# Kernel optimization log

Hardware: AMD Instinct MI355X
Metric: run time of the kernel (lower is better)

## Reference

```python
import jax, jax.numpy as jnp
import numpy as np

EMB = 64          # emb_size
LG = 64           # lg_msg_dim
NDB = 16          # num_dist_basis
NCB = 16          # num_cos_basis
NCLS = 40
NLAYERS = 2
NJK = NLAYERS + 2  # jumping-knowledge sequence length
HID = (NJK * EMB) // 2  # PyG JK-LSTM hidden size = 128


def setup_inputs() -> dict:
    key = jax.random.key(0)
    ks = jax.random.split(key, 24)
    N, Eg, Elg, F = 50000, 800000, 800000, 128
    s = 0.05
    inp = {
        "x": jax.random.normal(ks[0], (N, F), jnp.float32),
        "edge_index_g": jax.random.randint(ks[1], (2, Eg), 0, N, jnp.int32),
        "edge_attr_g": jax.random.uniform(ks[2], (Eg, NDB), jnp.float32),
        "edge_index_lg": jax.random.randint(ks[3], (2, Elg), 0, Eg, jnp.int32),
        "edge_attr_lg": jax.random.uniform(ks[4], (Elg, NCB), jnp.float32),
        # parameters (nn.Linear convention: W is [out, in])
        "W_feat": jax.random.normal(ks[5], (EMB, F), jnp.float32) * s,
        "W_msg": jax.random.normal(ks[6], (LG, 2 * EMB + NDB), jnp.float32) * s,
        "W_lg2g": jax.random.normal(ks[7], (EMB, LG), jnp.float32) * s,
        "b_lg2g": jax.random.normal(ks[8], (EMB,), jnp.float32) * s,
        "W_msg_layers": jax.random.normal(ks[9], (NLAYERS, LG, 2 * LG + NCB), jnp.float32) * s,
        # bidirectional LSTM params (PyTorch gate order i,f,g,o)
        "Wih_f": jax.random.normal(ks[10], (4 * HID, EMB), jnp.float32) * s,
        "Whh_f": jax.random.normal(ks[11], (4 * HID, HID), jnp.float32) * s,
        "bih_f": jax.random.normal(ks[12], (4 * HID,), jnp.float32) * s,
        "bhh_f": jax.random.normal(ks[13], (4 * HID,), jnp.float32) * s,
        "Wih_b": jax.random.normal(ks[14], (4 * HID, EMB), jnp.float32) * s,
        "Whh_b": jax.random.normal(ks[15], (4 * HID, HID), jnp.float32) * s,
        "bih_b": jax.random.normal(ks[16], (4 * HID,), jnp.float32) * s,
        "bhh_b": jax.random.normal(ks[17], (4 * HID,), jnp.float32) * s,
        "W_att": jax.random.normal(ks[18], (1, 2 * HID), jnp.float32) * s,
        "b_att": jax.random.normal(ks[19], (1,), jnp.float32) * s,
        "W_out": jax.random.normal(ks[20], (NCLS, EMB), jnp.float32) * s,
    }
    return inp


def _lstm(x_seq, Wih, Whh, bih, bhh, reverse):
    # x_seq: [N, L, C] -> hs: [N, L, H]
    N = x_seq.shape[0]
    H = Whh.shape[1]
    b = bih + bhh

    def step(carry, x_t):
        h, c = carry
        gates = x_t @ Wih.T + h @ Whh.T + b
        i, f, g, o = jnp.split(gates, 4, axis=-1)
        c = jax.nn.sigmoid(f) * c + jax.nn.sigmoid(i) * jnp.tanh(g)
        h = jax.nn.sigmoid(o) * jnp.tanh(c)
        return (h, c), h

    xs = jnp.swapaxes(x_seq, 0, 1)  # [L, N, C]
    init = (jnp.zeros((N, H), x_seq.dtype), jnp.zeros((N, H), x_seq.dtype))
    _, hs = jax.lax.scan(step, init, xs, reverse=reverse)
    return jnp.swapaxes(hs, 0, 1)


def reference(x, edge_index_g, edge_attr_g, edge_index_lg, edge_attr_lg,
              W_feat, W_msg, W_lg2g, b_lg2g, W_msg_layers,
              Wih_f, Whh_f, bih_f, bhh_f, Wih_b, Whh_b, bih_b, bhh_b,
              W_att, b_att, W_out):
    N = x.shape[0]
    Eg = edge_attr_g.shape[0]
    seg = jax.ops.segment_sum

    # node embedding (eval mode: dropout is identity)
    node_emb = jax.nn.relu(x @ W_feat.T)  # [N, EMB]

    # initial linegraph node features: gather endpoints -> concat -> linear -> relu
    m1 = node_emb[edge_index_g[0]]  # [Eg, EMB]
    m2 = node_emb[edge_index_g[1]]
    msg_emb = jax.nn.relu(jnp.concatenate([m1, m2, edge_attr_g], -1) @ W_msg.T)  # [Eg, LG]

    node_embs = [node_emb]
    msg_red = msg_emb @ W_lg2g.T + b_lg2g
    node_embs.append(seg(msg_red, edge_index_g[1], num_segments=N))

    # message-passing layers on the linegraph
    for l in range(W_msg_layers.shape[0]):
        s = msg_emb[edge_index_lg[0]]
        d = msg_emb[edge_index_lg[1]]
        m = jax.nn.relu(jnp.concatenate([s, d, edge_attr_lg], -1) @ W_msg_layers[l].T)
        msg_emb = seg(m, edge_index_lg[1], num_segments=Eg)  # scatter_add over linegraph
        incoming = seg(msg_emb, edge_index_g[1], num_segments=N)
        node_embs.append(incoming @ W_lg2g.T + b_lg2g)

    # JumpingKnowledge ('lstm'): bidirectional LSTM -> attention -> weighted sum
    x_jk = jnp.stack(node_embs, axis=1)  # [N, NJK, EMB]
    h_f = _lstm(x_jk, Wih_f, Whh_f, bih_f, bhh_f, reverse=False)
    h_b = _lstm(x_jk, Wih_b, Whh_b, bih_b, bhh_b, reverse=True)
    h = jnp.concatenate([h_f, h_b], -1)  # [N, NJK, 2*HID]
    alpha = jax.nn.softmax((h @ W_att.T + b_att)[..., 0], axis=-1)  # [N, NJK]
    final_emb = jnp.sum(x_jk * alpha[..., None], axis=1)  # [N, EMB]

    out = final_emb @ W_out.T
    return jax.nn.log_softmax(out, axis=-1)
```

## Files before the change

### kernel.cpp

```cpp
#include <hip/hip_runtime.h>

typedef unsigned short u16;
typedef unsigned int u32;
typedef __attribute__((ext_vector_type(8))) short bf16x8;
typedef __attribute__((ext_vector_type(4))) float f32x4;

#define MFMA(a, b, c) __builtin_amdgcn_mfma_f32_16x16x32_bf16(a, b, c, 0, 0, 0)

__device__ __forceinline__ u16 f2bf(float x) {
    union { float f; u32 u; } v; v.f = x;
    u32 r = (v.u + 0x7FFFu + ((v.u >> 16) & 1u)) >> 16;
    return (u16)r;
}
__device__ __forceinline__ float bf2f(u16 b) {
    union { u32 u; float f; } v; v.u = ((u32)b) << 16;
    return v.f;
}
__device__ __forceinline__ void casAddPair(u32* w, float lo, float hi) {
    u32 old = *w, assumed;
    do {
        assumed = old;
        u32 des = (u32)f2bf(bf2f((u16)(assumed & 0xFFFFu)) + lo) |
                  ((u32)f2bf(bf2f((u16)(assumed >> 16)) + hi) << 16);
        if (des == assumed) break;
        old = atomicCAS(w, assumed, des);
    } while (old != assumed);
}

__global__ __launch_bounds__(256) void prep_w(
    const float* __restrict__ Whh_f, const float* __restrict__ Whh_b,
    const float* __restrict__ Wih_f, const float* __restrict__ Wih_b,
    const float* __restrict__ bih_f, const float* __restrict__ bhh_f,
    const float* __restrict__ bih_b, const float* __restrict__ bhh_b,
    u16* __restrict__ WhhB, u16* __restrict__ WihB, float* __restrict__ BS)
{
    const float L2E = 1.4426950408889634f;
    int i = blockIdx.x * 256 + threadIdx.x;
    if (i < 131072) {
        int d = i >> 16, r = i & 65535;
        float s = (((r >> 14) & 3) == 2) ? 2.f * L2E : L2E;
        WhhB[i] = f2bf(s * (d ? Whh_b[r] : Whh_f[r]));
    } else if (i < 196608) {
        int i2 = i - 131072; int d = i2 >> 15, r = i2 & 32767;
        float s = (((r >> 13) & 3) == 2) ? 2.f * L2E : L2E;
        WihB[i2] = f2bf(s * (d ? Wih_b[r] : Wih_f[r]));
    } else if (i < 197632) {
        int i3 = i - 196608; int d = i3 >> 9, g = i3 & 511;
        float s = (((g >> 7) & 3) == 2) ? 2.f * L2E : L2E;
        BS[i3] = s * (d ? (bih_b[g] + bhh_b[g]) : (bih_f[g] + bhh_f[g]));
    }
}

__global__ __launch_bounds__(256) void count_kernel(const int* __restrict__ dst,
                                                    u32* __restrict__ cnt, long E)
{
    long i = (long)blockIdx.x * 256 + threadIdx.x;
    if (i < E) atomicAdd(&cnt[dst[i]], 1u);
}

__global__ __launch_bounds__(256) void scan1(const u32* __restrict__ a,
                                             u32* __restrict__ part, int n)
{
    __shared__ u32 ts[256];
    int b = blockIdx.x, t = threadIdx.x;
    long i0 = (long)b * 1024 + t * 4;
    u32 s = 0;
#pragma unroll
    for (int k = 0; k < 4; ++k) { long i = i0 + k; if (i < n) s += a[i]; }
    ts[t] = s; __syncthreads();
    for (int off = 1; off < 256; off <<= 1) {
        u32 x = (t >= off) ? ts[t - off] : 0u;
        __syncthreads(); ts[t] += x; __syncthreads();
    }
    if (t == 255) part[b] = ts[255];
}

__global__ __launch_bounds__(1024) void scan2(u32* __restrict__ part, int nb,
                                              u32* __restrict__ total_out)
{
    __shared__ u32 ts[1024];
    int t = threadIdx.x;
    u32 v = (t < nb) ? part[t] : 0u;
    ts[t] = v; __syncthreads();
    for (int off = 1; off < 1024; off <<= 1) {
        u32 x = (t >= off) ? ts[t - off] : 0u;
        __syncthreads(); ts[t] += x; __syncthreads();
    }
    if (t < nb) part[t] = ts[t] - v;
    if (t == 1023 && total_out) *total_out = ts[1023];
}

__global__ __launch_bounds__(256) void scan3(u32* __restrict__ a,
                                             const u32* __restrict__ part, int n)
{
    __shared__ u32 ts[256];
    int b = blockIdx.x, t = threadIdx.x;
    long i0 = (long)b * 1024 + t * 4;
    u32 v[4]; u32 s = 0;
#pragma unroll
    for (int k = 0; k < 4; ++k) { long i = i0 + k; v[k] = (i < n) ? a[i] : 0u; s += v[k]; }
    ts[t] = s; __syncthreads();
    for (int off = 1; off < 256; off <<= 1) {
        u32 x = (t >= off) ? ts[t - off] : 0u;
        __syncthreads(); ts[t] += x; __syncthreads();
    }
    u32 run = part[b] + ts[t] - s;
#pragma unroll
    for (int k = 0; k < 4; ++k) {
        long i = i0 + k;
        if (i < n) { u32 x = v[k]; a[i] = run; run += x; }
    }
}

__global__ __launch_bounds__(256) void fill_kernel(const int* __restrict__ dst,
                                                   u32* __restrict__ off,
                                                   int* __restrict__ list, long E)
{
    long i = (long)blockIdx.x * 256 + threadIdx.x;
    if (i < E) {
        u32 pos = atomicAdd(&off[dst[i]], 1u);
        list[pos] = (int)i;
    }
}

__global__ __launch_bounds__(256) void zero_fill(const u32* __restrict__ offc,
                                                 u16* __restrict__ outb, long NB)
{
    long idx = (long)blockIdx.x * 256 + threadIdx.x;
    long n = idx >> 3; int q = (int)(idx & 7);
    if (n >= NB) return;
    u32 s = n ? offc[n - 1] : 0u;
    u32 e = offc[n];
    bool need = (s == e) || ((s >> 7) != ((e - 1) >> 7));
    if (need) *(uint4*)(outb + n * 64 + q * 8) = make_uint4(0, 0, 0, 0);
}

template <int K, bool RELU, bool INBF16>
__global__ __launch_bounds__(256) void rowgemm(
    const void* __restrict__ in, const float* __restrict__ W,
    const float* __restrict__ bias, const float* __restrict__ bias_scale,
    u16* __restrict__ outb, int M)
{
    constexpr int KP = K + 8;
    __shared__ u16 inS[64 * KP];
    __shared__ u16 WS[64 * KP];
    int t = threadIdx.x;
    long rb = (long)blockIdx.x * 64;
    for (int i = t; i < 64 * K; i += 256) {
        int c = i / K, k = i - c * K;
        WS[c * KP + k] = f2bf(W[i]);
    }
    if (INBF16) {
        const u16* inb = (const u16*)in;
        for (int i = t; i < 64 * K / 8; i += 256) {
            int r = i / (K / 8), q = i - r * (K / 8);
            long gr = rb + r;
            uint4 v = make_uint4(0, 0, 0, 0);
            if (gr < M) v = *(const uint4*)&inb[gr * (long)K + q * 8];
            *(uint4*)&inS[r * KP + q * 8] = v;
        }
    } else {
        const float* inf = (const float*)in;
        for (int i = t; i < 64 * K; i += 256) {
            int r = i / K, k = i - r * K;
            long gr = rb + r;
            inS[r * KP + k] = (gr < M) ? f2bf(inf[gr * (long)K + k]) : (u16)0;
        }
    }
    __syncthreads();
    int l = t & 63, w = t >> 6, lr = l & 15, lq = l >> 4;
    f32x4 acc[4];
#pragma unroll
    for (int i = 0; i < 4; ++i) acc[i] = (f32x4){0.f, 0.f, 0.f, 0.f};
#pragma unroll
    for (int kc = 0; kc < K; kc += 32) {
        bf16x8 a = *(const bf16x8*)&inS[(w * 16 + lr) * KP + kc + lq * 8];
#pragma unroll
        for (int ct = 0; ct < 4; ++ct) {
            bf16x8 b = *(const bf16x8*)&WS[(ct * 16 + lr) * KP + kc + lq * 8];
            acc[ct] = MFMA(a, b, acc[ct]);
        }
    }
#pragma unroll
    for (int ct = 0; ct < 4; ++ct)
#pragma unroll
        for (int r = 0; r < 4; ++r) {
            long gr = rb + w * 16 + lq * 4 + r;
            if (gr < M) {
                int c = ct * 16 + lr;
                float v = acc[ct][r];
                if (bias) v += bias[c] * (bias_scale ? bias_scale[gr] : 1.f);
                if (RELU) v = fmaxf(v, 0.f);
                outb[gr * 64 + c] = f2bf(v);
            }
        }
}

__global__ __launch_bounds__(512, 4) void edge_msg_init2(
    const u16* __restrict__ feat, const int* __restrict__ ei,
    const float* __restrict__ attr, const float* __restrict__ W,
    u16* __restrict__ outb, long E)
{
    __shared__ u16 WS[64 * 168];
    __shared__ u16 eds[128 * 64];
    int t = threadIdx.x;
    long eb = (long)blockIdx.x * 128;
    for (int i = t; i < 64 * 144; i += 512) {
        int c = i / 144, k = i - c * 144;
        WS[c * 168 + k] = f2bf(W[i]);
    }
    for (int i = t; i < 64 * 24; i += 512) {
        int c = i / 24, k = 144 + (i - c * 24);
        WS[c * 168 + k] = 0;
    }
    int w = t >> 6, l = t & 63, lr = l & 15, lq = l >> 4;
    long e = eb + w * 16 + lr;
    long ec = (e < E) ? e : (E - 1);
    int src = ei[ec], dst = ei[E + ec];
    bf16x8 A[5];
    {
        const uint4* sp = (const uint4*)(feat + (long)src * 64);
        const uint4* dp = (const uint4*)(feat + (long)dst * 64);
        *(uint4*)&A[0] = sp[lq];
        *(uint4*)&A[1] = sp[4 + lq];
        *(uint4*)&A[2] = dp[lq];
        *(uint4*)&A[3] = dp[4 + lq];
        uint4 pv = make_uint4(0, 0, 0, 0);
        if (lq < 2) {
            const float4* ap = (const float4*)(attr + ec * 16) + lq * 2;
            float4 b0 = ap[0], b1 = ap[1];
            pv.x = (u32)f2bf(b0.x) | ((u32)f2bf(b0.y) << 16);
            pv.y = (u32)f2bf(b0.z) | ((u32)f2bf(b0.w) << 16);
            pv.z = (u32)f2bf(b1.x) | ((u32)f2bf(b1.y) << 16);
            pv.w = (u32)f2bf(b1.z) | ((u32)f2bf(b1.w) << 16);
        }
        *(uint4*)&A[4] = pv;
    }
    __syncthreads();
    f32x4 acc[4];
#pragma unroll
    for (int ct = 0; ct < 4; ++ct) acc[ct] = (f32x4){0.f, 0.f, 0.f, 0.f};
#pragma unroll
    for (int kc = 0; kc < 5; ++kc) {
#pragma unroll
        for (int ct = 0; ct < 4; ++ct) {
            bf16x8 b = *(const bf16x8*)&WS[(ct * 16 + lr) * 168 + kc * 32 + lq * 8];
            acc[ct] = MFMA(A[kc], b, acc[ct]);
        }
    }
#pragma unroll
    for (int ct = 0; ct < 4; ++ct)
#pragma unroll
        for (int r = 0; r < 4; ++r) {
            int row = w * 16 + lq * 4 + r;
            int col = ct * 16 + lr;
            eds[row * 64 + col] = f2bf(fmaxf(acc[ct][r], 0.f));
        }
    __syncthreads();
    for (int j = t; j < 1024; j += 512) {
        int le = j >> 3, q = j & 7;
        long e2 = eb + le;
        if (e2 < E)
            *(uint4*)(outb + e2 * 64 + q * 8) = *(const uint4*)&eds[le * 64 + q * 8];
    }
}

__global__ __launch_bounds__(512, 4) void edge_msg_lg2(
    const u16* __restrict__ feat, const int* __restrict__ ei,
    const float* __restrict__ attr, const float* __restrict__ W,
    const int* __restrict__ list, u16* __restrict__ outb, long E)
{
    __shared__ u16 WS[64 * 168];
    __shared__ u16 eds[128 * 64];
    __shared__ int dstS[128];
    __shared__ int idS[128];
    __shared__ int srcS[128];
    __shared__ int dprevS, dnextS;
    int t = threadIdx.x;
    long pb = (long)blockIdx.x * 128;
    for (int i = t; i < 64 * 144; i += 512) {
        int c = i / 144, k = i - c * 144;
        WS[c * 168 + k] = f2bf(W[i]);
    }
    for (int i = t; i < 64 * 24; i += 512) {
        int c = i / 24, k = 144 + (i - c * 24);
        WS[c * 168 + k] = 0;
    }
    if (t < 128) {
        long p = pb + t;
        int id = (p < E) ? list[p] : -1;
        idS[t] = id;
        srcS[t] = (id >= 0) ? ei[id] : 0;
        dstS[t] = (id >= 0) ? ei[E + id] : -1;
    } else if (t == 128) {
        dprevS = (pb > 0) ? ei[E + list[pb - 1]] : -2;
    } else if (t == 129) {
        dnextS = (pb + 128 < E) ? ei[E + list[pb + 128]] : -2;
    }
    __syncthreads();
    int w = t >> 6, l = t & 63, lr = l & 15, lq = l >> 4;
    int el = w * 16 + lr;
    int id = idS[el];
    long idc = (id >= 0) ? (long)id : 0;
    int src = srcS[el];
    int dst = (dstS[el] >= 0) ? dstS[el] : 0;
    bf16x8 A[5];
    {
        const uint4* sp = (const uint4*)(feat + (long)src * 64);
        const uint4* dp = (const uint4*)(feat + (long)dst * 64);
        *(uint4*)&A[0] = sp[lq];
        *(uint4*)&A[1] = sp[4 + lq];
        *(uint4*)&A[2] = dp[lq];
        *(uint4*)&A[3] = dp[4 + lq];
        uint4 pv = make_uint4(0, 0, 0, 0);
        if (lq < 2) {
            const float4* ap = (const float4*)(attr + idc * 16) + lq * 2;
            float4 b0 = ap[0], b1 = ap[1];
            pv.x = (u32)f2bf(b0.x) | ((u32)f2bf(b0.y) << 16);
            pv.y = (u32)f2bf(b0.z) | ((u32)f2bf(b0.w) << 16);
            pv.z = (u32)f2bf(b1.x) | ((u32)f2bf(b1.y) << 16);
            pv.w = (u32)f2bf(b1.z) | ((u32)f2bf(b1.w) << 16);
        }
        *(uint4*)&A[4] = pv;
    }
    f32x4 acc[4];
#pragma unroll
    for (int ct = 0; ct < 4; ++ct) acc[ct] = (f32x4){0.f, 0.f, 0.f, 0.f};
#pragma unroll
    for (int kc = 0; kc < 5; ++kc) {
#pragma unroll
        for (int ct = 0; ct < 4; ++ct) {
            bf16x8 b = *(const bf16x8*)&WS[(ct * 16 + lr) * 168 + kc * 32 + lq * 8];
            acc[ct] = MFMA(A[kc], b, acc[ct]);
        }
    }
#pragma unroll
    for (int ct = 0; ct < 4; ++ct)
#pragma unroll
        for (int r = 0; r < 4; ++r) {
            int row = w * 16 + lq * 4 + r;
            int col = ct * 16 + lr;
            eds[row * 64 + col] = f2bf(fmaxf(acc[ct][r], 0.f));
        }
    __syncthreads();
    for (int j = t; j < 4096; j += 512) {
        int le = j >> 5, wd = j & 31;
        int d = dstS[le];
        if (d < 0) continue;
        if (le > 0 && dstS[le - 1] == d) continue;
        float lo = 0.f, hi = 0.f;
        int le2 = le;
        do {
            u32 pair = *(const u32*)&eds[le2 * 64 + wd * 2];
            lo += bf2f((u16)(pair & 0xFFFFu));
            hi += bf2f((u16)(pair >> 16));
            ++le2;
        } while (le2 < 128 && dstS[le2] == d);
        bool bprev = (le == 0 && dprevS == d);
        bool bnext = (le2 == 128 && dnextS == d);
        u32* dw = (u32*)(outb + (long)d * 64 + wd * 2);
        if (bprev || bnext) {
            casAddPair(dw, lo, hi);
        } else {
            *dw = (u32)f2bf(lo) | ((u32)f2bf(hi) << 16);
        }
    }
}

__global__ __launch_bounds__(256) void gather_g(
    const u16* __restrict__ m, const int* __restrict__ list,
    const u32* __restrict__ offc, u16* __restrict__ aggB,
    float* __restrict__ degOut, int N)
{
    int t = threadIdx.x;
    int hw = t >> 5, c = t & 31;
    long n = (long)blockIdx.x * 8 + hw;
    if (n >= N) return;
    u32 start = n ? offc[n - 1] : 0u;
    u32 end = offc[n];
    float s0 = 0.f, s1 = 0.f;
    for (u32 i = start; i < end; ++i) {
        int e = list[i];
        u32 pair = *(const u32*)&m[(long)e * 64 + c * 2];
        s0 += bf2f((u16)(pair & 0xFFFFu));
        s1 += bf2f((u16)(pair >> 16));
    }
    *(u32*)&aggB[n * 64 + c * 2] = (u32)f2bf(s0) | ((u32)f2bf(s1) << 16);
    if (degOut && c == 0) degOut[n] = (float)(end - start);
}

__global__ __launch_bounds__(512, 2) void lstm3(
    const u16* __restrict__ jkB, const u16* __restrict__ WhhB,
    const u16* __restrict__ WihB, const float* __restrict__ BS,
    const float* __restrict__ Watt, float* __restrict__ scores,
    int N)
{
    __shared__ u16 hS[64 * 136];
    __shared__ u16 xS[4][64 * 72];
    __shared__ u16 WiS[512 * 72];
    __shared__ float bsS[512];
    __shared__ float part[4 * 64 * 8];
    int t = threadIdx.x;
    int dir = blockIdx.y;
    int w = t >> 6, l = t & 63, lr = l & 15, lq = l >> 4;
    const u16* WhhD = WhhB + (long)dir * 65536;
    const u16* WihD = WihB + (long)dir * 32768;
    long n0 = (long)blockIdx.x * 64;

    {
        int n = t >> 3, j = t & 7;
        long gn = n0 + n;
#pragma unroll
        for (int k = 0; k < 4; ++k) {
            uint4 v = make_uint4(0, 0, 0, 0);
            if (gn < N) v = *(const uint4*)&jkB[((long)k * N + gn) * 64 + j * 8];
            *(uint4*)&xS[k][n * 72 + j * 8] = v;
        }
    }
#pragma unroll
    for (int i = t; i < 4096; i += 512) {
        int g = i >> 3, q = i & 7;
        *(uint4*)&WiS[g * 72 + q * 8] = *(const uint4*)&WihD[g * 64 + q * 8];
    }
    bsS[t] = BS[dir * 512 + t];

    int grow0 = w * 16 + lq * 4;
    bf16x8 Wh[4][4];
#pragma unroll
    for (int ty = 0; ty < 4; ++ty) {
        int g = ty * 128 + w * 16 + lr;
#pragma unroll
        for (int kc = 0; kc < 4; ++kc)
            Wh[ty][kc] = *(const bf16x8*)&WhhD[g * 128 + kc * 32 + lq * 8];
    }
    float4 Wa4 = *(const float4*)&Watt[dir * 128 + grow0];
    float* scOut = scores + (long)dir * N * 4;

    float creg[4][4] = {};
    __syncthreads();

#pragma unroll 1
    for (int s = 0; s < 4; ++s) {
        int tt = dir ? (3 - s) : s;
        float u[4][4];
        {
            f32x4 acc[2][4];
            f32x4 bi = *(const f32x4*)&bsS[grow0];
            f32x4 bg = *(const f32x4*)&bsS[256 + grow0];
#pragma unroll
            for (int nt = 0; nt < 4; ++nt) { acc[0][nt] = bi; acc[1][nt] = bg; }
            if (s) {
#pragma unroll
                for (int kc = 0; kc < 4; ++kc) {
                    bf16x8 a[4];
#pragma unroll
                    for (int nt = 0; nt < 4; ++nt)
                        a[nt] = *(const bf16x8*)&hS[(nt * 16 + lr) * 136 + kc * 32 + lq * 8];
#pragma unroll
                    for (int nt = 0; nt < 4; ++nt) {
                        acc[0][nt] = MFMA(Wh[0][kc], a[nt], acc[0][nt]);
                        acc[1][nt] = MFMA(Wh[2][kc], a[nt], acc[1][nt]);
                    }
                }
            }
#pragma unroll
            for (int kc = 0; kc < 2; ++kc) {
                bf16x8 wi = *(const bf16x8*)&WiS[(w * 16 + lr) * 72 + kc * 32 + lq * 8];
                bf16x8 wg = *(const bf16x8*)&WiS[(256 + w * 16 + lr) * 72 + kc * 32 + lq * 8];
                bf16x8 a[4];
#pragma unroll
                for (int nt = 0; nt < 4; ++nt)
                    a[nt] = *(const bf16x8*)&xS[tt][(nt * 16 + lr) * 72 + kc * 32 + lq * 8];
#pragma unroll
                for (int nt = 0; nt < 4; ++nt) {
                    acc[0][nt] = MFMA(wi, a[nt], acc[0][nt]);
                    acc[1][nt] = MFMA(wg, a[nt], acc[1][nt]);
                }
            }
#pragma unroll
            for (int nt = 0; nt < 4; ++nt)
#pragma unroll
                for (int r = 0; r < 4; ++r) {
                    float si = __builtin_amdgcn_rcpf(
                        1.f + __builtin_amdgcn_exp2f(-acc[0][nt][r]));
                    float tg = 2.f * __builtin_amdgcn_rcpf(
                        1.f + __builtin_amdgcn_exp2f(-acc[1][nt][r])) - 1.f;
                    u[nt][r] = si * tg;
                }
        }
        {
            f32x4 acc[2][4];
            f32x4 bf = *(const f32x4*)&bsS[128 + grow0];
            f32x4 bo = *(const f32x4*)&bsS[384 + grow0];
#pragma unroll
            for (int nt = 0; nt < 4; ++nt) { acc[0][nt] = bf; acc[1][nt] = bo; }
            if (s) {
#pragma unroll
                for (int kc = 0; kc < 4; ++kc) {
                    bf16x8 a[4];
#pragma unroll
                    for (int nt = 0; nt < 4; ++nt)
                        a[nt] = *(const bf16x8*)&hS[(nt * 16 + lr) * 136 + kc * 32 + lq * 8];
#pragma unroll
                    for (int nt = 0; nt < 4; ++nt) {
                        acc[0][nt] = MFMA(Wh[1][kc], a[nt], acc[0][nt]);
                        acc[1][nt] = MFMA(Wh[3][kc], a[nt], acc[1][nt]);
                    }
                }
            }
#pragma unroll
            for (int kc = 0; kc < 2; ++kc) {
                bf16x8 wf = *(const bf16x8*)&WiS[(128 + w * 16 + lr) * 72 + kc * 32 + lq * 8];
                bf16x8 wo = *(const bf16x8*)&WiS[(384 + w * 16 + lr) * 72 + kc * 32 + lq * 8];
                bf16x8 a[4];
#pragma unroll
                for (int nt = 0; nt < 4; ++nt)
                    a[nt] = *(const bf16x8*)&xS[tt][(nt * 16 + lr) * 72 + kc * 32 + lq * 8];
#pragma unroll
                for (int nt = 0; nt < 4; ++nt) {
                    acc[0][nt] = MFMA(wf, a[nt], acc[0][nt]);
                    acc[1][nt] = MFMA(wo, a[nt], acc[1][nt]);
                }
            }
            if (s) __syncthreads();
#pragma unroll
            for (int nt = 0; nt < 4; ++nt) {
                float hv[4];
#pragma unroll
                for (int r = 0; r < 4; ++r) {
                    float sf = __builtin_amdgcn_rcpf(
                        1.f + __builtin_amdgcn_exp2f(-acc[0][nt][r]));
                    float c = sf * creg[nt][r] + u[nt][r];
                    float so = __builtin_amdgcn_rcpf(
                        1.f + __builtin_amdgcn_exp2f(-acc[1][nt][r]));
                    float th = 2.f * __builtin_amdgcn_rcpf(
                        1.f + __builtin_amdgcn_exp2f(-2.8853900817779268f * c)) - 1.f;
                    creg[nt][r] = c;
                    hv[r] = so * th;
                }
                float p = hv[0] * Wa4.x + hv[1] * Wa4.y + hv[2] * Wa4.z + hv[3] * Wa4.w;
                p += __shfl_xor(p, 16);
                p += __shfl_xor(p, 32);
                if (lq == 0) part[(tt * 64 + nt * 16 + lr) * 8 + w] = p;
                if (s < 3) {
                    u32 p0 = (u32)f2bf(hv[0]) | ((u32)f2bf(hv[1]) << 16);
                    u32 p1 = (u32)f2bf(hv[2]) | ((u32)f2bf(hv[3]) << 16);
                    *(uint2*)&hS[(nt * 16 + lr) * 136 + grow0] = make_uint2(p0, p1);
                }
            }
        }
        if (s < 3) __syncthreads();
    }
    __syncthreads();
    if (t < 256) {
        int tt = t >> 6, node = t & 63;
        long gn = n0 + node;
        if (gn < N) {
            const float4* pp = (const float4*)&part[(tt * 64 + node) * 8];
            float4 a = pp[0], b = pp[1];
            scOut[gn * 4 + tt] = a.x + a.y + a.z + a.w + b.x + b.y + b.z + b.w;
        }
    }
}

__global__ __launch_bounds__(256) void final_kernel(
    const u16* __restrict__ jkB, const float* __restrict__ scores,
    const float* __restrict__ Wout, float* __restrict__ out, int N)
{
    __shared__ float feS[4][64];
    int t = threadIdx.x, l = t & 63, w = t >> 6;
    long n = (long)blockIdx.x * 4 + w;
    bool ok = (n < N);
    long nn = ok ? n : (long)(N - 1);
    float sc[4];
#pragma unroll
    for (int tt = 0; tt < 4; ++tt)
        sc[tt] = scores[nn * 4 + tt] + scores[(long)N * 4 + nn * 4 + tt];
    float m = fmaxf(fmaxf(sc[0], sc[1]), fmaxf(sc[2], sc[3]));
    float e0 = __expf(sc[0] - m), e1 = __expf(sc[1] - m);
    float e2 = __expf(sc[2] - m), e3 = __expf(sc[3] - m);
    float den = e0 + e1 + e2 + e3;
    float a0 = e0 / den, a1 = e1 / den, a2 = e2 / den, a3 = e3 / den;
    float fe = a0 * bf2f(jkB[nn * 64 + l]) + a1 * bf2f(jkB[((long)N + nn) * 64 + l]) +
               a2 * bf2f(jkB[((long)2 * N + nn) * 64 + l]) +
               a3 * bf2f(jkB[((long)3 * N + nn) * 64 + l]);
    feS[w][l] = fe;
    __syncthreads();
    float logit = 0.f;
    if (l < 40)
        for (int c = 0; c < 64; ++c) logit += feS[w][c] * Wout[l * 64 + c];
    float v = (l < 40) ? logit : -1e30f;
    for (int off = 32; off; off >>= 1) v = fmaxf(v, __shfl_xor(v, off));
    float ex = (l < 40) ? __expf(logit - v) : 0.f;
    for (int off = 32; off; off >>= 1) ex += __shfl_xor(ex, off);
    if (ok && l < 40) out[n * 40 + l] = logit - v - __logf(ex);
}

extern "C" void kernel_launch(void* const* d_in, const int* in_sizes, int n_in,
                              void* d_out, int out_size, void* d_ws, size_t ws_size,
                              hipStream_t stream)
{
    const float* x        = (const float*)d_in[0];
    const int*   eig      = (const int*)d_in[1];
    const float* eag      = (const float*)d_in[2];
    const int*   eilg     = (const int*)d_in[3];
    const float* ealg     = (const float*)d_in[4];
    const float* W_feat   = (const float*)d_in[5];
    const float* W_msg    = (const float*)d_in[6];
    const float* W_lg2g   = (const float*)d_in[7];
    const float* b_lg2g   = (const float*)d_in[8];
    const float* W_msg_l  = (const float*)d_in[9];
    const float* Wih_f    = (const float*)d_in[10];
    const float* Whh_f    = (const float*)d_in[11];
    const float* bih_f    = (const float*)d_in[12];
    const float* bhh_f    = (const float*)d_in[13];
    const float* Wih_b    = (const float*)d_in[14];
    const float* Whh_b    = (const float*)d_in[15];
    const float* bih_b    = (const float*)d_in[16];
    const float* bhh_b    = (const float*)d_in[17];
    const float* W_att    = (const float*)d_in[18];
    const float* W_out    = (const float*)d_in[20];

    int  N   = in_sizes[0] / 128;
    long Eg  = in_sizes[1] / 2;
    long Elg = in_sizes[3] / 2;

    char* wp = (char*)d_ws;
    auto alloc = [&](size_t bytes) -> char* {
        char* p = wp; wp += (bytes + 255) & ~(size_t)255; return p;
    };
    u16*   jkB    = (u16*)  alloc((size_t)4 * N * 64 * 2);
    u16*   mA     = (u16*)  alloc((size_t)Eg * 64 * 2);
    u16*   mB     = (u16*)  alloc((size_t)Eg * 64 * 2);
    u16*   aggB   = (u16*)  alloc((size_t)N * 64 * 2);
    float* deg    = (float*)alloc((size_t)N * 4);
    float* scores = (float*)alloc((size_t)2 * N * 4 * 4);
    u16*   WhhB   = (u16*)  alloc((size_t)2 * 65536 * 2);
    u16*   WihB   = (u16*)  alloc((size_t)2 * 32768 * 2);
    float* BS     = (float*)alloc((size_t)2 * 512 * 4);
    u32*   off_g  = (u32*)  alloc((size_t)(N + 1) * 4);
    int*   list_g = (int*)  alloc((size_t)Eg * 4);
    u32*   off_lg = (u32*)  alloc((size_t)(Eg + 1) * 4);
    int*   list_lg= (int*)  alloc((size_t)Elg * 4);
    u32*   part   = (u32*)  alloc((size_t)1024 * 4);

    prep_w<<<772, 256, 0, stream>>>(Whh_f, Whh_b, Wih_f, Wih_b,
                                    bih_f, bhh_f, bih_b, bhh_b, WhhB, WihB, BS);
    hipMemsetAsync(off_g, 0, (size_t)(N + 1) * 4, stream);
    count_kernel<<<(int)((Eg + 255) / 256), 256, 0, stream>>>(eig + Eg, off_g, Eg);
    {
        int nb = (N + 1023) / 1024;
        scan1<<<nb, 256, 0, stream>>>(off_g, part, N);
        scan2<<<1, 1024, 0, stream>>>(part, nb, off_g + N);
        scan3<<<nb, 256, 0, stream>>>(off_g, part, N);
    }
    fill_kernel<<<(int)((Eg + 255) / 256), 256, 0, stream>>>(eig + Eg, off_g, list_g, Eg);
    hipMemsetAsync(off_lg, 0, (size_t)(Eg + 1) * 4, stream);
    count_kernel<<<(int)((Elg + 255) / 256), 256, 0, stream>>>(eilg + Elg, off_lg, Elg);
    {
        int nb = (int)((Eg + 1023) / 1024);
        scan1<<<nb, 256, 0, stream>>>(off_lg, part, (int)Eg);
        scan2<<<1, 1024, 0, stream>>>(part, nb, off_lg + Eg);
        scan3<<<nb, 256, 0, stream>>>(off_lg, part, (int)Eg);
    }
    fill_kernel<<<(int)((Elg + 255) / 256), 256, 0, stream>>>(eilg + Elg, off_lg, list_lg, Elg);

    rowgemm<128, true, false><<<(N + 63) / 64, 256, 0, stream>>>(
        x, W_feat, nullptr, nullptr, jkB, N);
    edge_msg_init2<<<(int)((Eg + 127) / 128), 512, 0, stream>>>(
        jkB, eig, eag, W_msg, mA, Eg);
    gather_g<<<(N + 7) / 8, 256, 0, stream>>>(mA, list_g, off_g, aggB, deg, N);
    rowgemm<64, false, true><<<(N + 63) / 64, 256, 0, stream>>>(
        aggB, W_lg2g, b_lg2g, deg, jkB + (size_t)N * 64, N);
    zero_fill<<<(int)((Eg * 8 + 255) / 256), 256, 0, stream>>>(off_lg, mB, Eg);
    edge_msg_lg2<<<(int)((Elg + 127) / 128), 512, 0, stream>>>(
        mA, eilg, ealg, W_msg_l, list_lg, mB, Elg);
    gather_g<<<(N + 7) / 8, 256, 0, stream>>>(mB, list_g, off_g, aggB, nullptr, N);
    rowgemm<64, false, true><<<(N + 63) / 64, 256, 0, stream>>>(
        aggB, W_lg2g, b_lg2g, nullptr, jkB + (size_t)2 * N * 64, N);
    zero_fill<<<(int)((Eg * 8 + 255) / 256), 256, 0, stream>>>(off_lg, mA, Eg);
    edge_msg_lg2<<<(int)((Elg + 127) / 128), 512, 0, stream>>>(
        mB, eilg, ealg, W_msg_l + 64 * 144, list_lg, mA, Elg);
    gather_g<<<(N + 7) / 8, 256, 0, stream>>>(mA, list_g, off_g, aggB, nullptr, N);
    rowgemm<64, false, true><<<(N + 63) / 64, 256, 0, stream>>>(
        aggB, W_lg2g, b_lg2g, nullptr, jkB + (size_t)3 * N * 64, N);
    {
        int ntiles = (N + 63) / 64;
        lstm3<<<dim3(ntiles, 2), 512, 0, stream>>>(
            jkB, WhhB, WihB, BS, W_att, scores, N);
    }
    final_kernel<<<(N + 3) / 4, 256, 0, stream>>>(
        jkB, scores, W_out, (float*)d_out, N);
}
```

Baseline: 1.061 ms.

## Pre-convert weights to bf16 once, split gather across two half-waves, slim LSTM LDS

Weight matrices for the feature, message and lg2g GEMMs are now converted to bf16 once in prep_w, and the edge and row GEMM kernels load them with vectorized 16-byte copies instead of converting fp32 per block. gather_g assigns one full wave per node, with each half-wave summing alternate edges before a shuffle reduction, which doubles parallelism on high-degree nodes. The LSTM kernel drops its input-weight and bias LDS staging, reads them from global or cache into registers, adds the biases before the activations, and raises the occupancy hint to 4. Packed bf16 conversion instructions replace the manual rounding, adding a few extra global loads per step in exchange.

```diff
diff --git a/kernel.cpp b/kernel.cpp
--- a/kernel.cpp
+++ b/kernel.cpp
@@ -32,7 +32,11 @@
     const float* __restrict__ Wih_f, const float* __restrict__ Wih_b,
     const float* __restrict__ bih_f, const float* __restrict__ bhh_f,
     const float* __restrict__ bih_b, const float* __restrict__ bhh_b,
-    u16* __restrict__ WhhB, u16* __restrict__ WihB, float* __restrict__ BS)
+    const float* __restrict__ W_feat, const float* __restrict__ W_msg,
+    const float* __restrict__ W_msg_l, const float* __restrict__ W_lg2g,
+    u16* __restrict__ WhhB, u16* __restrict__ WihB, float* __restrict__ BS,
+    u16* __restrict__ WfeatB, u16* __restrict__ WmsgB,
+    u16* __restrict__ WmsgLB, u16* __restrict__ Wlg2gB)
 {
     const float L2E = 1.4426950408889634f;
     int i = blockIdx.x * 256 + threadIdx.x;
@@ -48,6 +52,14 @@
         int i3 = i - 196608; int d = i3 >> 9, g = i3 & 511;
         float s = (((g >> 7) & 3) == 2) ? 2.f * L2E : L2E;
         BS[i3] = s * (d ? (bih_b[g] + bhh_b[g]) : (bih_f[g] + bhh_f[g]));
+    } else if (i < 205824) {
+        int j = i - 197632; WfeatB[j] = f2bf(W_feat[j]);
+    } else if (i < 215040) {
+        int j = i - 205824; WmsgB[j] = f2bf(W_msg[j]);
+    } else if (i < 233472) {
+        int j = i - 215040; WmsgLB[j] = f2bf(W_msg_l[j]);
+    } else if (i < 237568) {
+        int j = i - 233472; Wlg2gB[j] = f2bf(W_lg2g[j]);
     }
 }
 
@@ -137,23 +149,24 @@
 
 template <int K, bool RELU, bool INBF16>
 __global__ __launch_bounds__(256) void rowgemm(
-    const void* __restrict__ in, const float* __restrict__ W,
+    const void* __restrict__ in, const u16* __restrict__ W,
     const float* __restrict__ bias, const float* __restrict__ bias_scale,
     u16* __restrict__ outb, int M)
 {
     constexpr int KP = K + 8;
+    constexpr int K8 = K / 8;
     __shared__ u16 inS[64 * KP];
     __shared__ u16 WS[64 * KP];
     int t = threadIdx.x;
     long rb = (long)blockIdx.x * 64;
-    for (int i = t; i < 64 * K; i += 256) {
-        int c = i / K, k = i - c * K;
-        WS[c * KP + k] = f2bf(W[i]);
+    for (int i = t; i < 64 * K8; i += 256) {
+        int c = i / K8, q = i - c * K8;
+        *(uint4*)&WS[c * KP + q * 8] = *(const uint4*)&W[c * K + q * 8];
     }
     if (INBF16) {
         const u16* inb = (const u16*)in;
-        for (int i = t; i < 64 * K / 8; i += 256) {
-            int r = i / (K / 8), q = i - r * (K / 8);
+        for (int i = t; i < 64 * K8; i += 256) {
+            int r = i / K8, q = i - r * K8;
             long gr = rb + r;
             uint4 v = make_uint4(0, 0, 0, 0);
             if (gr < M) v = *(const uint4*)&inb[gr * (long)K + q * 8];
@@ -198,20 +211,20 @@
 
 __global__ __launch_bounds__(512, 4) void edge_msg_init2(
     const u16* __restrict__ feat, const int* __restrict__ ei,
-    const float* __restrict__ attr, const float* __restrict__ W,
+    const float* __restrict__ attr, const u16* __restrict__ W,
     u16* __restrict__ outb, long E)
 {
     __shared__ u16 WS[64 * 168];
     __shared__ u16 eds[128 * 64];
     int t = threadIdx.x;
     long eb = (long)blockIdx.x * 128;
-    for (int i = t; i < 64 * 144; i += 512) {
-        int c = i / 144, k = i - c * 144;
-        WS[c * 168 + k] = f2bf(W[i]);
-    }
-    for (int i = t; i < 64 * 24; i += 512) {
-        int c = i / 24, k = 144 + (i - c * 24);
-        WS[c * 168 + k] = 0;
+    for (int i = t; i < 1152; i += 512) {
+        int c = i / 18, q = i - c * 18;
+        *(uint4*)&WS[c * 168 + q * 8] = *(const uint4*)&W[c * 144 + q * 8];
+    }
+    if (t < 192) {
+        int c = t / 3, q = t - c * 3;
+        *(uint4*)&WS[c * 168 + 144 + q * 8] = make_uint4(0, 0, 0, 0);
     }
     int w = t >> 6, l = t & 63, lr = l & 15, lq = l >> 4;
     long e = eb + w * 16 + lr;
@@ -267,7 +280,7 @@
 
 __global__ __launch_bounds__(512, 4) void edge_msg_lg2(
     const u16* __restrict__ feat, const int* __restrict__ ei,
-    const float* __restrict__ attr, const float* __restrict__ W,
+    const float* __restrict__ attr, const u16* __restrict__ W,
     const int* __restrict__ list, u16* __restrict__ outb, long E)
 {
     __shared__ u16 WS[64 * 168];
@@ -278,13 +291,13 @@
     __shared__ int dprevS, dnextS;
     int t = threadIdx.x;
     long pb = (long)blockIdx.x * 128;
-    for (int i = t; i < 64 * 144; i += 512) {
-        int c = i / 144, k = i - c * 144;
-        WS[c * 168 + k] = f2bf(W[i]);
-    }
-    for (int i = t; i < 64 * 24; i += 512) {
-        int c = i / 24, k = 144 + (i - c * 24);
-        WS[c * 168 + k] = 0;
+    for (int i = t; i < 1152; i += 512) {
+        int c = i / 18, q = i - c * 18;
+        *(uint4*)&WS[c * 168 + q * 8] = *(const uint4*)&W[c * 144 + q * 8];
+    }
+    if (t < 192) {
+        int c = t / 3, q = t - c * 3;
+        *(uint4*)&WS[c * 168 + 144 + q * 8] = make_uint4(0, 0, 0, 0);
     }
     if (t < 128) {
         long p = pb + t;
@@ -373,23 +386,26 @@
     float* __restrict__ degOut, int N)
 {
     int t = threadIdx.x;
-    int hw = t >> 5, c = t & 31;
-    long n = (long)blockIdx.x * 8 + hw;
+    int wv = t >> 6, c = t & 31, half = (t >> 5) & 1;
+    long n = (long)blockIdx.x * 4 + wv;
     if (n >= N) return;
     u32 start = n ? offc[n - 1] : 0u;
     u32 end = offc[n];
     float s0 = 0.f, s1 = 0.f;
-    for (u32 i = start; i < end; ++i) {
+    for (u32 i = start + half; i < end; i += 2) {
         int e = list[i];
         u32 pair = *(const u32*)&m[(long)e * 64 + c * 2];
         s0 += bf2f((u16)(pair & 0xFFFFu));
         s1 += bf2f((u16)(pair >> 16));
     }
-    *(u32*)&aggB[n * 64 + c * 2] = (u32)f2bf(s0) | ((u32)f2bf(s1) << 16);
-    if (degOut && c == 0) degOut[n] = (float)(end - start);
-}
-
-__global__ __launch_bounds__(512, 2) void lstm3(
+    s0 += __shfl_xor(s0, 32);
+    s1 += __shfl_xor(s1, 32);
+    if (half == 0)
+        *(u32*)&aggB[n * 64 + c * 2] = (u32)f2bf(s0) | ((u32)f2bf(s1) << 16);
+    if (degOut && c == 0 && half == 0) degOut[n] = (float)(end - start);
+}
+
+__global__ __launch_bounds__(512, 4) void lstm3(
     const u16* __restrict__ jkB, const u16* __restrict__ WhhB,
     const u16* __restrict__ WihB, const float* __restrict__ BS,
     const float* __restrict__ Watt, float* __restrict__ scores,
@@ -397,8 +413,6 @@
 {
     __shared__ u16 hS[64 * 136];
     __shared__ u16 xS[4][64 * 72];
-    __shared__ u16 WiS[512 * 72];
-    __shared__ float bsS[512];
     __shared__ float part[4 * 64 * 8];
     int t = threadIdx.x;
     int dir = blockIdx.y;
@@ -417,12 +431,6 @@
             *(uint4*)&xS[k][n * 72 + j * 8] = v;
         }
     }
-#pragma unroll
-    for (int i = t; i < 4096; i += 512) {
-        int g = i >> 3, q = i & 7;
-        *(uint4*)&WiS[g * 72 + q * 8] = *(const uint4*)&WihD[g * 64 + q * 8];
-    }
-    bsS[t] = BS[dir * 512 + t];
 
     int grow0 = w * 16 + lq * 4;
     bf16x8 Wh[4][4];
@@ -433,6 +441,8 @@
         for (int kc = 0; kc < 4; ++kc)
             Wh[ty][kc] = *(const bf16x8*)&WhhD[g * 128 + kc * 32 + lq * 8];
     }
+    const u16* pWiBase = WihD + (w * 16 + lr) * 64 + lq * 8;
+    const float* pBBase = BS + dir * 512 + grow0;
     float4 Wa4 = *(const float4*)&Watt[dir * 128 + grow0];
     float* scOut = scores + (long)dir * N * 4;
 
@@ -442,13 +452,23 @@
 #pragma unroll 1
     for (int s = 0; s < 4; ++s) {
         int tt = dir ? (3 - s) : s;
+        const u16* pW = pWiBase;
+        const float* pBp = pBBase;
+        asm volatile("" : "+v"(pW), "+v"(pBp));
         float u[4][4];
         {
+            bf16x8 wi0 = *(const bf16x8*)(pW);
+            bf16x8 wi1 = *(const bf16x8*)(pW + 32);
+            bf16x8 wg0 = *(const bf16x8*)(pW + 16384);
+            bf16x8 wg1 = *(const bf16x8*)(pW + 16416);
+            f32x4 bi = *(const f32x4*)(pBp);
+            f32x4 bg = *(const f32x4*)(pBp + 256);
             f32x4 acc[2][4];
-            f32x4 bi = *(const f32x4*)&bsS[grow0];
-            f32x4 bg = *(const f32x4*)&bsS[256 + grow0];
-#pragma unroll
-            for (int nt = 0; nt < 4; ++nt) { acc[0][nt] = bi; acc[1][nt] = bg; }
+#pragma unroll
+            for (int nt = 0; nt < 4; ++nt) {
+                acc[0][nt] = (f32x4){0.f, 0.f, 0.f, 0.f};
+                acc[1][nt] = (f32x4){0.f, 0.f, 0.f, 0.f};
+            }
             if (s) {
 #pragma unroll
                 for (int kc = 0; kc < 4; ++kc) {
@@ -465,8 +485,8 @@
             }
 #pragma unroll
             for (int kc = 0; kc < 2; ++kc) {
-                bf16x8 wi = *(const bf16x8*)&WiS[(w * 16 + lr) * 72 + kc * 32 + lq * 8];
-                bf16x8 wg = *(const bf16x8*)&WiS[(256 + w * 16 + lr) * 72 + kc * 32 + lq * 8];
+                bf16x8 wi = kc ? wi1 : wi0;
+                bf16x8 wg = kc ? wg1 : wg0;
                 bf16x8 a[4];
 #pragma unroll
                 for (int nt = 0; nt < 4; ++nt)
@@ -482,18 +502,25 @@
 #pragma unroll
                 for (int r = 0; r < 4; ++r) {
                     float si = __builtin_amdgcn_rcpf(
-                        1.f + __builtin_amdgcn_exp2f(-acc[0][nt][r]));
+                        1.f + __builtin_amdgcn_exp2f(-(acc[0][nt][r] + bi[r])));
                     float tg = 2.f * __builtin_amdgcn_rcpf(
-                        1.f + __builtin_amdgcn_exp2f(-acc[1][nt][r])) - 1.f;
+                        1.f + __builtin_amdgcn_exp2f(-(acc[1][nt][r] + bg[r]))) - 1.f;
                     u[nt][r] = si * tg;
                 }
         }
         {
+            bf16x8 wf0 = *(const bf16x8*)(pW + 8192);
+            bf16x8 wf1 = *(const bf16x8*)(pW + 8224);
+            bf16x8 wo0 = *(const bf16x8*)(pW + 24576);
+            bf16x8 wo1 = *(const bf16x8*)(pW + 24608);
+            f32x4 bfv = *(const f32x4*)(pBp + 128);
+            f32x4 bov = *(const f32x4*)(pBp + 384);
             f32x4 acc[2][4];
-            f32x4 bf = *(const f32x4*)&bsS[128 + grow0];
-            f32x4 bo = *(const f32x4*)&bsS[384 + grow0];
-#pragma unroll
-            for (int nt = 0; nt < 4; ++nt) { acc[0][nt] = bf; acc[1][nt] = bo; }
+#pragma unroll
+            for (int nt = 0; nt < 4; ++nt) {
+                acc[0][nt] = (f32x4){0.f, 0.f, 0.f, 0.f};
+                acc[1][nt] = (f32x4){0.f, 0.f, 0.f, 0.f};
+            }
             if (s) {
 #pragma unroll
                 for (int kc = 0; kc < 4; ++kc) {
@@ -510,8 +537,8 @@
             }
 #pragma unroll
             for (int kc = 0; kc < 2; ++kc) {
-                bf16x8 wf = *(const bf16x8*)&WiS[(128 + w * 16 + lr) * 72 + kc * 32 + lq * 8];
-                bf16x8 wo = *(const bf16x8*)&WiS[(384 + w * 16 + lr) * 72 + kc * 32 + lq * 8];
+                bf16x8 wf = kc ? wf1 : wf0;
+                bf16x8 wo = kc ? wo1 : wo0;
                 bf16x8 a[4];
 #pragma unroll
                 for (int nt = 0; nt < 4; ++nt)
@@ -529,10 +556,10 @@
 #pragma unroll
                 for (int r = 0; r < 4; ++r) {
                     float sf = __builtin_amdgcn_rcpf(
-                        1.f + __builtin_amdgcn_exp2f(-acc[0][nt][r]));
+                        1.f + __builtin_amdgcn_exp2f(-(acc[0][nt][r] + bfv[r])));
                     float c = sf * creg[nt][r] + u[nt][r];
                     float so = __builtin_amdgcn_rcpf(
-                        1.f + __builtin_amdgcn_exp2f(-acc[1][nt][r]));
+                        1.f + __builtin_amdgcn_exp2f(-(acc[1][nt][r] + bov[r])));
                     float th = 2.f * __builtin_amdgcn_rcpf(
                         1.f + __builtin_amdgcn_exp2f(-2.8853900817779268f * c)) - 1.f;
                     creg[nt][r] = c;
@@ -543,8 +570,9 @@
                 p += __shfl_xor(p, 32);
                 if (lq == 0) part[(tt * 64 + nt * 16 + lr) * 8 + w] = p;
                 if (s < 3) {
-                    u32 p0 = (u32)f2bf(hv[0]) | ((u32)f2bf(hv[1]) << 16);
-                    u32 p1 = (u32)f2bf(hv[2]) | ((u32)f2bf(hv[3]) << 16);
+                    u32 p0, p1;
+                    asm("v_cvt_pk_bf16_f32 %0, %1, %2" : "=v"(p0) : "v"(hv[0]), "v"(hv[1]));
+                    asm("v_cvt_pk_bf16_f32 %0, %1, %2" : "=v"(p1) : "v"(hv[2]), "v"(hv[3]));
                     *(uint2*)&hS[(nt * 16 + lr) * 136 + grow0] = make_uint2(p0, p1);
                 }
             }
@@ -638,14 +666,21 @@
     u16*   WhhB   = (u16*)  alloc((size_t)2 * 65536 * 2);
     u16*   WihB   = (u16*)  alloc((size_t)2 * 32768 * 2);
     float* BS     = (float*)alloc((size_t)2 * 512 * 4);
+    u16*   WfeatB = (u16*)  alloc((size_t)8192 * 2);
+    u16*   WmsgB  = (u16*)  alloc((size_t)9216 * 2);
+    u16*   WmsgLB = (u16*)  alloc((size_t)18432 * 2);
+    u16*   Wlg2gB = (u16*)  alloc((size_t)4096 * 2);
     u32*   off_g  = (u32*)  alloc((size_t)(N + 1) * 4);
     int*   list_g = (int*)  alloc((size_t)Eg * 4);
     u32*   off_lg = (u32*)  alloc((size_t)(Eg + 1) * 4);
     int*   list_lg= (int*)  alloc((size_t)Elg * 4);
     u32*   part   = (u32*)  alloc((size_t)1024 * 4);
 
-    prep_w<<<772, 256, 0, stream>>>(Whh_f, Whh_b, Wih_f, Wih_b,
-                                    bih_f, bhh_f, bih_b, bhh_b, WhhB, WihB, BS);
+    prep_w<<<928, 256, 0, stream>>>(Whh_f, Whh_b, Wih_f, Wih_b,
+                                    bih_f, bhh_f, bih_b, bhh_b,
+                                    W_feat, W_msg, W_msg_l, W_lg2g,
+                                    WhhB, WihB, BS,
+                                    WfeatB, WmsgB, WmsgLB, Wlg2gB);
     hipMemsetAsync(off_g, 0, (size_t)(N + 1) * 4, stream);
     count_kernel<<<(int)((Eg + 255) / 256), 256, 0, stream>>>(eig + Eg, off_g, Eg);
     {
@@ -666,24 +701,24 @@
     fill_kernel<<<(int)((Elg + 255) / 256), 256, 0, stream>>>(eilg + Elg, off_lg, list_lg, Elg);
 
     rowgemm<128, true, false><<<(N + 63) / 64, 256, 0, stream>>>(
-        x, W_feat, nullptr, nullptr, jkB, N);
+        x, WfeatB, nullptr, nullptr, jkB, N);
     edge_msg_init2<<<(int)((Eg + 127) / 128), 512, 0, stream>>>(
-        jkB, eig, eag, W_msg, mA, Eg);
-    gather_g<<<(N + 7) / 8, 256, 0, stream>>>(mA, list_g, off_g, aggB, deg, N);
+        jkB, eig, eag, WmsgB, mA, Eg);
+    gather_g<<<(N + 3) / 4, 256, 0, stream>>>(mA, list_g, off_g, aggB, deg, N);
     rowgemm<64, false, true><<<(N + 63) / 64, 256, 0, stream>>>(
-        aggB, W_lg2g, b_lg2g, deg, jkB + (size_t)N * 64, N);
+        aggB, Wlg2gB, b_lg2g, deg, jkB + (size_t)N * 64, N);
     zero_fill<<<(int)((Eg * 8 + 255) / 256), 256, 0, stream>>>(off_lg, mB, Eg);
     edge_msg_lg2<<<(int)((Elg + 127) / 128), 512, 0, stream>>>(
-        mA, eilg, ealg, W_msg_l, list_lg, mB, Elg);
-    gather_g<<<(N + 7) / 8, 256, 0, stream>>>(mB, list_g, off_g, aggB, nullptr, N);
+        mA, eilg, ealg, WmsgLB, list_lg, mB, Elg);
+    gather_g<<<(N + 3) / 4, 256, 0, stream>>>(mB, list_g, off_g, aggB, nullptr, N);
     rowgemm<64, false, true><<<(N + 63) / 64, 256, 0, stream>>>(
-        aggB, W_lg2g, b_lg2g, nullptr, jkB + (size_t)2 * N * 64, N);
+        aggB, Wlg2gB, b_lg2g, nullptr, jkB + (size_t)2 * N * 64, N);
     zero_fill<<<(int)((Eg * 8 + 255) / 256), 256, 0, stream>>>(off_lg, mA, Eg);
     edge_msg_lg2<<<(int)((Elg + 127) / 128), 512, 0, stream>>>(
-        mB, eilg, ealg, W_msg_l + 64 * 144, list_lg, mA, Elg);
-    gather_g<<<(N + 7) / 8, 256, 0, stream>>>(mA, list_g, off_g, aggB, nullptr, N);
+        mB, eilg, ealg, WmsgLB + 9216, list_lg, mA, Elg);
+    gather_g<<<(N + 3) / 4, 256, 0, stream>>>(mA, list_g, off_g, aggB, nullptr, N);
     rowgemm<64, false, true><<<(N + 63) / 64, 256, 0, stream>>>(
-        aggB, W_lg2g, b_lg2g, nullptr, jkB + (size_t)3 * N * 64, N);
+        aggB, Wlg2gB, b_lg2g, nullptr, jkB + (size_t)3 * N * 64, N);
     {
         int ntiles = (N + 63) / 64;
         lstm3<<<dim3(ntiles, 2), 512, 0, stream>>>(
```

Result: slower. 1.185 ms (+11.7%).
